# Optimization experiments

Hardware: AMD Instinct MI355X
Metric: run time of the kernel (lower is better)

The kernel has to match this reference:

```python
import jax, jax.numpy as jnp
import numpy as np

# MORRConfig_20um_MQ ring parameters
A = 0.8578   # attenuation factor a
R = 0.8985   # coupling factor r

IN_C, OUT_C, KS, STRIDE, PAD, MB = 32, 64, 3, 1, 1, 8
WIN = IN_C * KS * KS                      # 288 = kernel_size^2 * in_channel
WIN_PAD = ((WIN + MB - 1) // MB) * MB     # padded to multiple of miniblock
OUT_PAD = ((OUT_C + MB - 1) // MB) * MB
Q = WIN_PAD // MB                         # grid_dim_x = 36
P = OUT_PAD // MB                         # grid_dim_y = 8
MORR_GAIN = (100.0 / (WIN // MB)) ** 0.5  # input power normalization


def mrr_tr(phi):
    # all-pass MORR roundtrip-phase -> transmission intensity
    # T = (a^2 - 2ar cos(phi) + r^2) / (1 - 2ar cos(phi) + (ar)^2)
    c = 2.0 * A * R * jnp.cos(phi)
    return (A * A + R * R - c) / (1.0 + (A * R) ** 2 - c)


def im2col(x):
    # torch F.unfold ordering: feature dim ordered (C, ki, kj)
    B, C, H, W = x.shape
    xp = jnp.pad(x, ((0, 0), (0, 0), (PAD, PAD), (PAD, PAD)))
    Ho = (H + 2 * PAD - KS) // STRIDE + 1
    Wo = (W + 2 * PAD - KS) // STRIDE + 1
    cols = [xp[:, :, i:i + Ho * STRIDE:STRIDE, j:j + Wo * STRIDE:STRIDE]
            for i in range(KS) for j in range(KS)]
    p = jnp.stack(cols, axis=2)               # [B, C, KS*KS, Ho, Wo]
    return p.reshape(B, C * KS * KS, Ho * Wo), Ho, Wo


def setup_inputs() -> dict:
    key = jax.random.key(0)
    k1, k2, k3 = jax.random.split(key, 3)
    x = jax.random.uniform(k1, (8, IN_C, 64, 64), dtype=jnp.float32)  # intensity-encoded, nonneg
    weight = jax.random.uniform(k2, (P, Q, MB), dtype=jnp.float32) * 0.2  # nonneg MORR weights
    morr_output_scale = jax.random.normal(k3, (max(1, Q // 2) + 1,), dtype=jnp.float32) * 0.1
    return {"x": x, "weight": weight, "morr_output_scale": morr_output_scale}


def reference(x, weight, morr_output_scale):
    B = x.shape[0]
    cols, Ho, Wo = im2col(x)
    xb = cols.transpose(0, 2, 1)
    if WIN_PAD > WIN:
        xb = jnp.pad(xb, ((0, 0), (0, 0), (0, WIN_PAD - WIN)))
    xb = xb.reshape(-1, Q, MB)                # [Bs, Q, MB]
    inten = (xb * xb) * MORR_GAIN             # optical intensity (power-normalized)

    # block-circulant weighted phase accumulation == circular conv per (p,q) block, via rFFT
    Wf = jnp.fft.rfft(weight, axis=-1)        # [P, Q, MBf]
    Xf = jnp.fft.rfft(inten, axis=-1)         # [Bs, Q, MBf]
    phase = jnp.fft.irfft(Xf[:, None, :, :] * Wf[None], n=MB, axis=-1)  # [Bs, P, Q, MB]

    tr = mrr_tr(phase)                        # MORR nonlinear transfer

    # differential rails: learnable balancing factor per block-column pair (+1 pad scale)
    half = morr_output_scale[:-1]             # [Q//2]
    if Q % 2 == 0:
        scale = jnp.concatenate([half, -half])                              # [Q]
    else:
        scale = jnp.concatenate([half, morr_output_scale[-1:], -half])      # [Q]

    out = jnp.einsum("bpqk,q->bpk", tr, scale).reshape(-1, OUT_PAD)[:, :OUT_C]
    out = out.reshape(B, Ho * Wo, OUT_C).transpose(0, 2, 1).reshape(B, OUT_C, Ho, Wo)
    return out
```

## Files before the change

### kernel.cpp

```cpp
#include <hip/hip_runtime.h>

#define THREADS 256

#define IN_C 32
#define OUT_C 64
#define HW 64
#define Q_N 36
#define P_N 8
#define MB 8

#define SXPLANE 102
#define W2SZ (Q_N * P_N * MB)

__global__ __launch_bounds__(THREADS, 4)
void morr_conv_kernel(const float* __restrict__ x,
                      const float* __restrict__ weight,
                      const float* __restrict__ mos,
                      float* __restrict__ out)
{
    __shared__ float sx[IN_C * SXPLANE];
    __shared__ float w2[W2SZ];
    __shared__ float slds[Q_N];

    const int tid = threadIdx.x;
    const int blk = blockIdx.x;
    const int b   = blk >> 7;
    const int tile = blk & 127;
    const int row = tile >> 1;
    const int w0  = (tile & 1) << 5;

    const float GAIN    = 1.6666666666666667f;
    const float INV2PI  = 0.15915494309189535f;

    for (int idx = tid; idx < IN_C * SXPLANE; idx += THREADS) {
        int c   = idx / SXPLANE;
        int rem = idx - c * SXPLANE;
        int r   = rem / 34;
        int col = rem - r * 34;
        int gh = row + r - 1;
        int gw = w0 + col - 1;
        float v = 0.f;
        if ((unsigned)gh < 64u && (unsigned)gw < 64u)
            v = x[((b * IN_C + c) * HW + gh) * HW + gw];
        sx[idx] = GAIN * v * v;
    }
    for (int idx = tid; idx < W2SZ; idx += THREADS) {
        int p   = idx / (Q_N * MB);
        int rem = idx - p * (Q_N * MB);
        int q   = rem >> 3;
        int m   = idx & 7;
        w2[(q * P_N + p) * MB + m] = weight[idx] * INV2PI;
    }
    if (tid < Q_N)
        slds[tid] = (tid < 18) ? mos[tid] : -mos[tid - 18];
    __syncthreads();

    const int px = tid & 31;
    const int p  = tid >> 5;

    const float A_ = 0.8578f, R_ = 0.8985f;
    const float S_ = A_ * A_ + R_ * R_;
    const float D_ = 1.f + (A_ * R_) * (A_ * R_);
    const float C2 = 2.f * A_ * R_;
    const float E_ = S_ - D_;

    float acc[8];
#pragma unroll
    for (int i = 0; i < 8; ++i) acc[i] = 0.f;

    const float4* w4 = (const float4*)w2;

#pragma unroll 1
    for (int z = 0; z < 4; ++z) {
        const int sbase = (z * 8) * SXPLANE + px;
        const int qz = z * 9;
#pragma unroll
        for (int qi = 0; qi < 9; ++qi) {
            float iv[8];
#pragma unroll
            for (int j = 0; j < 8; ++j) {
                const int u  = qi * 8 + j;
                const int cu = u / 9;
                const int r  = u - cu * 9;
                const int ki = r / 3;
                const int kj = r - ki * 3;
                iv[j] = sx[sbase + cu * SXPLANE + ki * 34 + kj];
            }
            const float sc = slds[qz + qi];
            const int wq = ((qz + qi) * P_N + p) * 2;
            float4 wlo = w4[wq], whi = w4[wq + 1];
            float wv[8] = {wlo.x, wlo.y, wlo.z, wlo.w, whi.x, whi.y, whi.z, whi.w};

            float ph[8];
#pragma unroll
            for (int k = 0; k < 8; ++k) ph[k] = iv[0] * wv[k];
#pragma unroll
            for (int j = 1; j < 8; ++j) {
#pragma unroll
                for (int k = 0; k < 8; ++k)
                    ph[k] = fmaf(iv[j], wv[(k - j) & 7], ph[k]);
            }
#pragma unroll
            for (int k = 0; k < 8; ++k) {
                float cc = __builtin_amdgcn_cosf(ph[k]);
                float d  = fmaf(-C2, cc, D_);
                float r_ = __builtin_amdgcn_rcpf(d);
                acc[k] = fmaf(sc, r_, acc[k]);
            }
        }
    }

    float* op = out + ((b * OUT_C + p * MB) * (HW * HW)) + row * HW + w0 + px;
#pragma unroll
    for (int k = 0; k < 8; ++k)
        op[k * (HW * HW)] = E_ * acc[k];
}

extern "C" void kernel_launch(void* const* d_in, const int* in_sizes, int n_in,
                              void* d_out, int out_size, void* d_ws, size_t ws_size,
                              hipStream_t stream) {
    const float* x      = (const float*)d_in[0];
    const float* weight = (const float*)d_in[1];
    const float* mos    = (const float*)d_in[2];
    float* out = (float*)d_out;

    dim3 grid(1024), block(THREADS);
    hipLaunchKernelGGL(morr_conv_kernel, grid, block, 0, stream, x, weight, mos, out);
}
```

Baseline: 96.11 us.

## Split output channels across thread halves and halve pixel tile width

Each block now covers 16 pixels instead of 32, and the two halves of the block each compute 4 of the 8 output channels of a miniblock, using a rotated weight load so the circulant index still works. The grid doubles, per-thread accumulators and phase registers shrink, and launch bounds allow 8 blocks per CU for higher occupancy. The E_ constant is folded into the per-q scale. In exchange the halo overhead of the shared input tile is larger and the im2col values are loaded once per 4 outputs instead of per 8, so there is more LDS traffic per output.

```diff
diff --git a/kernel.cpp b/kernel.cpp
--- a/kernel.cpp
+++ b/kernel.cpp
@@ -9,34 +9,42 @@
 #define P_N 8
 #define MB 8
 
-#define SXPLANE 102
+#define TPX 16
+#define SXW 18
+#define SXSZ (IN_C * 3 * SXW)
 #define W2SZ (Q_N * P_N * MB)
 
-__global__ __launch_bounds__(THREADS, 4)
+__global__ __launch_bounds__(THREADS, 8)
 void morr_conv_kernel(const float* __restrict__ x,
                       const float* __restrict__ weight,
                       const float* __restrict__ mos,
                       float* __restrict__ out)
 {
-    __shared__ float sx[IN_C * SXPLANE];
+    __shared__ float sx[SXSZ];
     __shared__ float w2[W2SZ];
     __shared__ float slds[Q_N];
 
     const int tid = threadIdx.x;
     const int blk = blockIdx.x;
-    const int b   = blk >> 7;
-    const int tile = blk & 127;
-    const int row = tile >> 1;
-    const int w0  = (tile & 1) << 5;
+    const int b    = blk >> 8;
+    const int rem  = blk & 255;
+    const int row  = rem >> 2;
+    const int w0   = (rem & 3) << 4;
 
-    const float GAIN    = 1.6666666666666667f;
-    const float INV2PI  = 0.15915494309189535f;
+    const float GAIN   = 1.6666666666666667f;
+    const float INV2PI = 0.15915494309189535f;
 
-    for (int idx = tid; idx < IN_C * SXPLANE; idx += THREADS) {
-        int c   = idx / SXPLANE;
-        int rem = idx - c * SXPLANE;
-        int r   = rem / 34;
-        int col = rem - r * 34;
+    const float A_ = 0.8578f, R_ = 0.8985f;
+    const float S_ = A_ * A_ + R_ * R_;
+    const float D_ = 1.f + (A_ * R_) * (A_ * R_);
+    const float C2 = 2.f * A_ * R_;
+    const float E_ = S_ - D_;
+
+    for (int idx = tid; idx < SXSZ; idx += THREADS) {
+        int c    = idx / (3 * SXW);
+        int rem2 = idx - c * (3 * SXW);
+        int r    = rem2 / SXW;
+        int col  = rem2 - r * SXW;
         int gh = row + r - 1;
         int gw = w0 + col - 1;
         float v = 0.f;
@@ -45,34 +53,29 @@
         sx[idx] = GAIN * v * v;
     }
     for (int idx = tid; idx < W2SZ; idx += THREADS) {
-        int p   = idx / (Q_N * MB);
-        int rem = idx - p * (Q_N * MB);
-        int q   = rem >> 3;
-        int m   = idx & 7;
+        int p    = idx / (Q_N * MB);
+        int rem2 = idx - p * (Q_N * MB);
+        int q    = rem2 >> 3;
+        int m    = idx & 7;
         w2[(q * P_N + p) * MB + m] = weight[idx] * INV2PI;
     }
     if (tid < Q_N)
-        slds[tid] = (tid < 18) ? mos[tid] : -mos[tid - 18];
+        slds[tid] = ((tid < 18) ? mos[tid] : -mos[tid - 18]) * E_;
     __syncthreads();
 
-    const int px = tid & 31;
-    const int p  = tid >> 5;
+    const int px = tid & 15;
+    const int p  = (tid >> 4) & 7;
+    const int kh = tid >> 7;
 
-    const float A_ = 0.8578f, R_ = 0.8985f;
-    const float S_ = A_ * A_ + R_ * R_;
-    const float D_ = 1.f + (A_ * R_) * (A_ * R_);
-    const float C2 = 2.f * A_ * R_;
-    const float E_ = S_ - D_;
-
-    float acc[8];
+    float acc[4];
 #pragma unroll
-    for (int i = 0; i < 8; ++i) acc[i] = 0.f;
+    for (int i = 0; i < 4; ++i) acc[i] = 0.f;
 
     const float4* w4 = (const float4*)w2;
 
 #pragma unroll 1
     for (int z = 0; z < 4; ++z) {
-        const int sbase = (z * 8) * SXPLANE + px;
+        const int sbase = (z * 8) * (3 * SXW) + px;
         const int qz = z * 9;
 #pragma unroll
         for (int qi = 0; qi < 9; ++qi) {
@@ -84,36 +87,37 @@
                 const int r  = u - cu * 9;
                 const int ki = r / 3;
                 const int kj = r - ki * 3;
-                iv[j] = sx[sbase + cu * SXPLANE + ki * 34 + kj];
+                iv[j] = sx[sbase + cu * (3 * SXW) + ki * SXW + kj];
             }
             const float sc = slds[qz + qi];
+
             const int wq = ((qz + qi) * P_N + p) * 2;
-            float4 wlo = w4[wq], whi = w4[wq + 1];
-            float wv[8] = {wlo.x, wlo.y, wlo.z, wlo.w, whi.x, whi.y, whi.z, whi.w};
+            float4 wa = w4[wq + kh];
+            float4 wb = w4[wq + 1 - kh];
+            float wv[8] = {wa.x, wa.y, wa.z, wa.w, wb.x, wb.y, wb.z, wb.w};
 
-            float ph[8];
+            float ph[4];
 #pragma unroll
-            for (int k = 0; k < 8; ++k) ph[k] = iv[0] * wv[k];
+            for (int kk = 0; kk < 4; ++kk) ph[kk] = iv[0] * wv[kk];
 #pragma unroll
             for (int j = 1; j < 8; ++j) {
 #pragma unroll
-                for (int k = 0; k < 8; ++k)
-                    ph[k] = fmaf(iv[j], wv[(k - j) & 7], ph[k]);
+                for (int kk = 0; kk < 4; ++kk)
+                    ph[kk] = fmaf(iv[j], wv[(kk - j) & 7], ph[kk]);
             }
 #pragma unroll
-            for (int k = 0; k < 8; ++k) {
-                float cc = __builtin_amdgcn_cosf(ph[k]);
+            for (int kk = 0; kk < 4; ++kk) {
+                float cc = __builtin_amdgcn_cosf(ph[kk]);
                 float d  = fmaf(-C2, cc, D_);
-                float r_ = __builtin_amdgcn_rcpf(d);
-                acc[k] = fmaf(sc, r_, acc[k]);
+                acc[kk] = fmaf(sc, __builtin_amdgcn_rcpf(d), acc[kk]);
             }
         }
     }
 
-    float* op = out + ((b * OUT_C + p * MB) * (HW * HW)) + row * HW + w0 + px;
+    float* op = out + ((b * OUT_C + p * MB + kh * 4) * (HW * HW)) + row * HW + w0 + px;
 #pragma unroll
-    for (int k = 0; k < 8; ++k)
-        op[k * (HW * HW)] = E_ * acc[k];
+    for (int kk = 0; kk < 4; ++kk)
+        op[kk * (HW * HW)] = acc[kk];
 }
 
 extern "C" void kernel_launch(void* const* d_in, const int* in_sizes, int n_in,
@@ -124,6 +128,6 @@
     const float* mos    = (const float*)d_in[2];
     float* out = (float*)d_out;
 
-    dim3 grid(1024), block(THREADS);
+    dim3 grid(2048), block(THREADS);
     hipLaunchKernelGGL(morr_conv_kernel, grid, block, 0, stream, x, weight, mos, out);
 }
```

Result: faster. 91.23 us (-5.1%).

## Use full-row tiles with 512 threads and read weights via scalar loads

Applied to the files above, without the earlier changes.

Each block now covers a full 64-pixel output row with 512 threads (8 wavefronts, one per output group p), so the grid halves to 512 blocks and the halo overhead in the staged input tile shrinks. Weights are no longer staged in LDS. They are read directly from global memory through a wave-uniform pointer, so the compiler can use scalar loads. The 1/2π and GAIN factors are folded into the input staging, and E is folded into the output scales, which removes a multiply per output. The risks are lower occupancy from larger blocks, possible LDS bank conflicts with the 66-wide stride, and fewer blocks to spread across the CUs.

```diff
diff --git a/kernel.cpp b/kernel.cpp
--- a/kernel.cpp
+++ b/kernel.cpp
@@ -1,6 +1,6 @@
 #include <hip/hip_runtime.h>
 
-#define THREADS 256
+#define THREADS 512
 
 #define IN_C 32
 #define OUT_C 64
@@ -9,8 +9,9 @@
 #define P_N 8
 #define MB 8
 
-#define SXPLANE 102
-#define W2SZ (Q_N * P_N * MB)
+#define SXW 66
+#define SXPL (3 * SXW)
+#define SXSZ (IN_C * SXPL)
 
 __global__ __launch_bounds__(THREADS, 4)
 void morr_conv_kernel(const float* __restrict__ x,
@@ -18,45 +19,15 @@
                       const float* __restrict__ mos,
                       float* __restrict__ out)
 {
-    __shared__ float sx[IN_C * SXPLANE];
-    __shared__ float w2[W2SZ];
+    __shared__ float sx[SXSZ];
     __shared__ float slds[Q_N];
 
     const int tid = threadIdx.x;
     const int blk = blockIdx.x;
-    const int b   = blk >> 7;
-    const int tile = blk & 127;
-    const int row = tile >> 1;
-    const int w0  = (tile & 1) << 5;
+    const int b   = blk >> 6;
+    const int row = blk & 63;
 
-    const float GAIN    = 1.6666666666666667f;
-    const float INV2PI  = 0.15915494309189535f;
-
-    for (int idx = tid; idx < IN_C * SXPLANE; idx += THREADS) {
-        int c   = idx / SXPLANE;
-        int rem = idx - c * SXPLANE;
-        int r   = rem / 34;
-        int col = rem - r * 34;
-        int gh = row + r - 1;
-        int gw = w0 + col - 1;
-        float v = 0.f;
-        if ((unsigned)gh < 64u && (unsigned)gw < 64u)
-            v = x[((b * IN_C + c) * HW + gh) * HW + gw];
-        sx[idx] = GAIN * v * v;
-    }
-    for (int idx = tid; idx < W2SZ; idx += THREADS) {
-        int p   = idx / (Q_N * MB);
-        int rem = idx - p * (Q_N * MB);
-        int q   = rem >> 3;
-        int m   = idx & 7;
-        w2[(q * P_N + p) * MB + m] = weight[idx] * INV2PI;
-    }
-    if (tid < Q_N)
-        slds[tid] = (tid < 18) ? mos[tid] : -mos[tid - 18];
-    __syncthreads();
-
-    const int px = tid & 31;
-    const int p  = tid >> 5;
+    const float GI = 1.6666666666666667f * 0.15915494309189535f;
 
     const float A_ = 0.8578f, R_ = 0.8985f;
     const float S_ = A_ * A_ + R_ * R_;
@@ -64,16 +35,35 @@
     const float C2 = 2.f * A_ * R_;
     const float E_ = S_ - D_;
 
+    for (int idx = tid; idx < SXSZ; idx += THREADS) {
+        int c    = idx / SXPL;
+        int rem  = idx - c * SXPL;
+        int r    = rem / SXW;
+        int col  = rem - r * SXW;
+        int gh = row + r - 1;
+        int gw = col - 1;
+        float v = 0.f;
+        if ((unsigned)gh < 64u && (unsigned)gw < 64u)
+            v = x[((b * IN_C + c) * HW + gh) * HW + gw];
+        sx[idx] = GI * v * v;
+    }
+    if (tid < Q_N)
+        slds[tid] = ((tid < 18) ? mos[tid] : -mos[tid - 18]) * E_;
+    __syncthreads();
+
+    const int px = tid & 63;
+    const int p  = __builtin_amdgcn_readfirstlane(tid >> 6);
+    const float* __restrict__ wp = weight + p * (Q_N * MB);
+
     float acc[8];
 #pragma unroll
     for (int i = 0; i < 8; ++i) acc[i] = 0.f;
 
-    const float4* w4 = (const float4*)w2;
-
 #pragma unroll 1
     for (int z = 0; z < 4; ++z) {
-        const int sbase = (z * 8) * SXPLANE + px;
+        const int sbase = (z * 8) * SXPL + px;
         const int qz = z * 9;
+        const float* __restrict__ wpz = wp + z * 9 * MB;
 #pragma unroll
         for (int qi = 0; qi < 9; ++qi) {
             float iv[8];
@@ -84,12 +74,11 @@
                 const int r  = u - cu * 9;
                 const int ki = r / 3;
                 const int kj = r - ki * 3;
-                iv[j] = sx[sbase + cu * SXPLANE + ki * 34 + kj];
+                iv[j] = sx[sbase + cu * SXPL + ki * SXW + kj];
             }
-            const float sc = slds[qz + qi];
-            const int wq = ((qz + qi) * P_N + p) * 2;
-            float4 wlo = w4[wq], whi = w4[wq + 1];
-            float wv[8] = {wlo.x, wlo.y, wlo.z, wlo.w, whi.x, whi.y, whi.z, whi.w};
+            float wv[8];
+#pragma unroll
+            for (int m = 0; m < 8; ++m) wv[m] = wpz[qi * MB + m];
 
             float ph[8];
 #pragma unroll
@@ -100,20 +89,20 @@
                 for (int k = 0; k < 8; ++k)
                     ph[k] = fmaf(iv[j], wv[(k - j) & 7], ph[k]);
             }
+            const float sc = slds[qz + qi];
 #pragma unroll
             for (int k = 0; k < 8; ++k) {
                 float cc = __builtin_amdgcn_cosf(ph[k]);
                 float d  = fmaf(-C2, cc, D_);
-                float r_ = __builtin_amdgcn_rcpf(d);
-                acc[k] = fmaf(sc, r_, acc[k]);
+                acc[k] = fmaf(sc, __builtin_amdgcn_rcpf(d), acc[k]);
             }
         }
     }
 
-    float* op = out + ((b * OUT_C + p * MB) * (HW * HW)) + row * HW + w0 + px;
+    float* op = out + ((b * OUT_C + p * MB) * (HW * HW)) + row * HW + px;
 #pragma unroll
     for (int k = 0; k < 8; ++k)
-        op[k * (HW * HW)] = E_ * acc[k];
+        op[k * (HW * HW)] = acc[k];
 }
 
 extern "C" void kernel_launch(void* const* d_in, const int* in_sizes, int n_in,
@@ -124,6 +113,6 @@
     const float* mos    = (const float*)d_in[2];
     float* out = (float*)d_out;
 
-    dim3 grid(1024), block(THREADS);
+    dim3 grid(512), block(THREADS);
     hipLaunchKernelGGL(morr_conv_kernel, grid, block, 0, stream, x, weight, mos, out);
 }
```

New measurement: 92.97 us. -3.3%, faster.
